# Performance work log

Hardware: AMD Instinct MI355X
Metric: run time of the kernel (lower is better)

The kernel has to match this reference:

```python
import jax, jax.numpy as jnp
import numpy as np

NUM_MODES = 64
BATCH = 512


def calc_tensor(num_modes: int) -> np.ndarray:
    # Kronecker-delta selection-rule coupling tensor, shape [M, M, M, M]
    v = np.arange(1, num_modes + 1)
    m, i, j, k = np.meshgrid(v, v, v, v, indexing='ij')
    d = lambda a, b: (a == b).astype(np.int64)
    B = i * j * k ** 2 * (
        d(k + i, m + j) - d(k + i, -(m + j))
        + d(k + i, m - j) - d(k + i, -(m - j))
        + d(k - i, m + j) - d(k - i, -(m + j))
        + d(k - i, m - j) - d(k - i, -(m - j))
    )
    A = 0.5 * np.pi ** 4 * (B + np.transpose(B, (0, 3, 1, 2)) + np.transpose(B, (0, 2, 3, 1)))
    return A.astype(np.float32)


def setup_inputs() -> dict:
    key = jax.random.key(0)
    q = jax.random.normal(key, (BATCH, NUM_MODES), dtype=jnp.float32)
    A = jnp.asarray(calc_tensor(NUM_MODES))  # [M, M, M, M], fixed buffer
    return {"q": q, "A": A}


def reference(q, A):
    # original: q_vec = einsum('bm,bn,bk->mnkb', q, q, q).flatten -> [M^3, B];
    # out = -(A_flat @ q_vec).T  ==  -einsum('mijk,bi,bj,bk->bm', A, q, q, q)
    return -jnp.einsum('mijk,bi,bj,bk->bm', A, q, q, q)
```

## Files before the change

kernel.cpp:

```cpp
#include <hip/hip_runtime.h>


__global__ __launch_bounds__(64) void nsf_kernel(const float* __restrict__ q,
                                                 float* __restrict__ out) {
    const int b = blockIdx.x;
    const int t = threadIdx.x;

    __shared__ float u[64];
    __shared__ float w[64];
    __shared__ float Es[256];

    const float qv = q[b * 64 + t];
    const float fi = (float)(t + 1);
    u[t] = fi * qv;
    w[t] = fi * fi * qv;
    __syncthreads();

    #pragma unroll
    for (int rep = 0; rep < 2; ++rep) {
        const int s = t + 1 + rep * 64;
        float acc = 0.f;
        const int ilo = (s - 64 > 1) ? (s - 64) : 1;
        const int ihi = (s - 1 < 64) ? (s - 1) : 64;
        for (int i = ilo; i <= ihi; ++i) acc += u[i - 1] * w[s - i - 1];
        for (int k = s + 1; k <= 64; ++k) acc += u[k - s - 1] * w[k - 1];
        for (int k = 1; k <= 64 - s; ++k) acc -= u[k + s - 1] * w[k - 1];
        Es[127 + s] = acc;
        if (s <= 127) Es[127 - s] = -acc;
    }
    if (t == 0) Es[127] = 0.f;
    __syncthreads();

    const int m = t + 1;
    float acc = 0.f;
    #pragma unroll 8
    for (int j = 1; j <= 64; ++j) {
        acc += u[j - 1] * (Es[127 + m + j] + Es[127 + m - j]);
    }
    const float kconst = -146.11363655100363f;
    out[b * 64 + t] = kconst * acc;
}

extern "C" void kernel_launch(void* const* d_in, const int* in_sizes, int n_in,
                              void* d_out, int out_size, void* d_ws, size_t ws_size,
                              hipStream_t stream) {
    const float* q = (const float*)d_in[0];
    float* out = (float*)d_out;
    const int batch = in_sizes[0] / 64;
    nsf_kernel<<<batch, 64, 0, stream>>>(q, out);
}
```

Before: 96.13 us.

## Replace branchy correlation loops with zero-padded shared arrays and a fixed trip count

The variable-bound correlation loops for E are replaced by a single 64-iteration loop that reads zero-padded and mirrored shared-memory copies of u. Every thread now has the same trip count, which removes divergence and the per-thread bounds computation. The final reduction loop is fully unrolled. The cost is extra shared memory, extra initialization stores, and some multiplies by padded zeros.

```diff
diff --git a/kernel.cpp b/kernel.cpp
--- a/kernel.cpp
+++ b/kernel.cpp
@@ -6,36 +6,46 @@
     const int b = blockIdx.x;
     const int t = threadIdx.x;
 
-    __shared__ float u[64];
     __shared__ float w[64];
+    __shared__ float Ue[192];
+    __shared__ float Up[256];
     __shared__ float Es[256];
 
     const float qv = q[b * 64 + t];
     const float fi = (float)(t + 1);
-    u[t] = fi * qv;
+    const float uv = fi * qv;
+
+    Ue[128 + t] = 0.f;
+    Up[65 + t]  = 0.f;
+    Up[129 + t] = 0.f;
+    if (t == 0) { Ue[63] = 0.f; Up[0] = 0.f; }
+
     w[t] = fi * fi * qv;
+    Up[t + 1] = uv;
+    Ue[64 + t] = uv;
+    if (t <= 62) Ue[62 - t] = uv;
     __syncthreads();
 
+    const int s0 = t + 1;
+    float acc0 = 0.f, acc1 = 0.f;
     #pragma unroll
-    for (int rep = 0; rep < 2; ++rep) {
-        const int s = t + 1 + rep * 64;
-        float acc = 0.f;
-        const int ilo = (s - 64 > 1) ? (s - 64) : 1;
-        const int ihi = (s - 1 < 64) ? (s - 1) : 64;
-        for (int i = ilo; i <= ihi; ++i) acc += u[i - 1] * w[s - i - 1];
-        for (int k = s + 1; k <= 64; ++k) acc += u[k - s - 1] * w[k - 1];
-        for (int k = 1; k <= 64 - s; ++k) acc -= u[k + s - 1] * w[k - 1];
-        Es[127 + s] = acc;
-        if (s <= 127) Es[127 - s] = -acc;
+    for (int k = 1; k <= 64; ++k) {
+        const float wk = w[k - 1];
+        acc0 += wk * (Ue[63 + s0 - k] - Up[k + s0]);
+        acc1 += wk * Ue[127 + s0 - k];
     }
+    Es[127 + s0] = acc0;
+    Es[127 - s0] = -acc0;
+    Es[191 + s0] = acc1;
+    if (s0 <= 63) Es[63 - s0] = -acc1;
     if (t == 0) Es[127] = 0.f;
     __syncthreads();
 
     const int m = t + 1;
     float acc = 0.f;
-    #pragma unroll 8
+    #pragma unroll
     for (int j = 1; j <= 64; ++j) {
-        acc += u[j - 1] * (Es[127 + m + j] + Es[127 + m - j]);
+        acc += Up[j] * (Es[127 + m + j] + Es[127 + m - j]);
     }
     const float kconst = -146.11363655100363f;
     out[b * 64 + t] = kconst * acc;
```

Result: faster. 89.10 us (-7.3%).
